# Performance work log

Hardware: AMD Instinct MI355X
Metric: run time of the kernel (lower is better)

The kernel has to match this reference:

```python
import jax, jax.numpy as jnp
import numpy as np

N = 50000   # nodes
E = 800000  # edges (before self-loops)
IN = 256    # in_dim
H = 4       # heads
C = 64      # out_dim per head
NEG_SLOPE = 0.2
BN_EPS = 1e-5


def setup_inputs() -> dict:
    key = jax.random.key(0)
    ks = jax.random.split(key, 6)
    feature = jax.random.normal(ks[0], (N, IN), jnp.float32)
    edge_index = jax.random.randint(ks[1], (2, E), 0, N, dtype=jnp.int64)
    W = jax.random.normal(ks[2], (IN, H * C), jnp.float32) * 0.05
    att_src = jax.random.normal(ks[3], (H, C), jnp.float32) * 0.1
    att_dst = jax.random.normal(ks[4], (H, C), jnp.float32) * 0.1
    bias = jnp.zeros((H * C,), jnp.float32)
    gamma = jnp.ones((H * C,), jnp.float32)
    beta = jnp.zeros((H * C,), jnp.float32)
    return {"feature": feature, "edge_index": edge_index, "W": W,
            "att_src": att_src, "att_dst": att_dst, "bias": bias,
            "gamma": gamma, "beta": beta}


def reference(feature, edge_index, W, att_src, att_dst, bias, gamma, beta):
    n = feature.shape[0]
    # linear projection -> [N, H, C]
    x = (feature @ W).reshape(n, H, C)
    # per-node attention logits [N, H]
    a_src = jnp.einsum('nhc,hc->nh', x, att_src)
    a_dst = jnp.einsum('nhc,hc->nh', x, att_dst)
    # add self loops (PyG GATConv default)
    loop = jnp.arange(n, dtype=edge_index.dtype)
    src = jnp.concatenate([edge_index[0], loop])
    dst = jnp.concatenate([edge_index[1], loop])
    # edge attention scores [E+N, H]
    e = jax.nn.leaky_relu(a_src[src] + a_dst[dst], NEG_SLOPE)
    # segment softmax over incoming edges of each dst node
    m = jax.ops.segment_max(e, dst, num_segments=n)
    ex = jnp.exp(e - m[dst])
    denom = jax.ops.segment_sum(ex, dst, num_segments=n)
    alpha = ex / denom[dst]                       # [E+N, H]
    # weighted message aggregation -> [N, H, C]
    msg = x[src] * alpha[:, :, None]
    out = jax.ops.segment_sum(msg, dst, num_segments=n)
    h = out.reshape(n, H * C) + bias
    # batchnorm over nodes (training-mode batch statistics)
    mu = jnp.mean(h, axis=0)
    var = jnp.var(h, axis=0)
    h = (h - mu) * jax.lax.rsqrt(var + BN_EPS) * gamma + beta
    # ELU activation
    h = jax.nn.elu(h)
    # residual (in_dim == out_dim * num_heads)
    return feature + h
```

## Files before the change

### kernel.cpp

```cpp
#include <hip/hip_runtime.h>

#define N_NODES 50000
#define N_EDGES 800000
#define NEG_SLOPE 0.2f
#define BN_EPS  1e-5f
#define LOG2E   1.44269504088896f

#define CHUNKS 256
#define EDGES_PER_CHUNK 3125
#define NCOARSE 1024
#define NBUCKET 782
#define GEMM_BLOCKS 782

typedef short bf16x8 __attribute__((ext_vector_type(8)));
typedef float floatx4 __attribute__((ext_vector_type(4)));

__device__ inline ushort f2bf(float f) {
    union { float f; unsigned u; } v; v.f = f;
    unsigned r = v.u + 0x7fff + ((v.u >> 16) & 1);
    return (ushort)(r >> 16);
}
__device__ inline float bf2f(ushort h) {
    union { unsigned u; float f; } v; v.u = ((unsigned)h) << 16;
    return v.f;
}

__global__ __launch_bounds__(256) void count_wt_kernel(const int* __restrict__ ei,
                                                       const float* __restrict__ W,
                                                       int* __restrict__ counts,
                                                       ushort* __restrict__ Wtb,
                                                       float* __restrict__ bnacc)
{
    __shared__ int hist[NCOARSE];
    const int t = threadIdx.x;
    const int b = blockIdx.x;
    if (b < CHUNKS) {
        for (int j = t; j < NCOARSE; j += 256) hist[j] = 0;
        __syncthreads();
        const int e0 = b * EDGES_PER_CHUNK;
        for (int e = e0 + t; e < e0 + EDGES_PER_CHUNK; e += 256)
            atomicAdd(&hist[ei[N_EDGES + e] >> 6], 1);
        __syncthreads();
        for (int j = t; j < NCOARSE; j += 256)
            counts[j * CHUNKS + b] = hist[j];
    } else {
        const int n = b - CHUNKS;
        Wtb[n * 256 + t] = f2bf(W[t * 256 + n]);
        if (n < 16) bnacc[n * 256 + t] = 0.f;
    }
}

__global__ __launch_bounds__(256) void sscan1_kernel(int* __restrict__ counts,
                                                     int* __restrict__ blocksum)
{
    __shared__ int sm[256];
    const int t = threadIdx.x;
    const int i = blockIdx.x * 256 + t;
    const int v = counts[i];
    sm[t] = v;
    __syncthreads();
#pragma unroll
    for (int off = 1; off < 256; off <<= 1) {
        const int u = (t >= off) ? sm[t - off] : 0;
        __syncthreads();
        sm[t] += u;
        __syncthreads();
    }
    counts[i] = sm[t] - v;
    if (t == 255) blocksum[blockIdx.x] = sm[255];
}

#define LDSTRIDE 40
__global__ __launch_bounds__(256) void scatter_gemm_kernel(const int* __restrict__ ei,
                                                           const int* __restrict__ counts,
                                                           const int* __restrict__ blocksum,
                                                           int* __restrict__ blockbase,
                                                           uint* __restrict__ tmp,
                                                           const float* __restrict__ A,
                                                           const ushort* __restrict__ Bt,
                                                           const float* __restrict__ att_src,
                                                           const float* __restrict__ att_dst,
                                                           ushort* __restrict__ Xb,
                                                           float* __restrict__ s,
                                                           float* __restrict__ d)
{
    __shared__ __align__(16) char smem[25600];
    const int tid = threadIdx.x;

    if (blockIdx.x < CHUNKS) {
        int* sm     = (int*)smem;
        int* bbase  = sm + 256;
        int* cursor = bbase + NCOARSE;
        const int t = tid;
        const int blk = blockIdx.x;

        int v[4], loc[4], tot = 0;
#pragma unroll
        for (int j = 0; j < 4; ++j) {
            v[j] = blocksum[t * 4 + j];
            loc[j] = tot;
            tot += v[j];
        }
        sm[t] = tot;
        __syncthreads();
#pragma unroll
        for (int off = 1; off < 256; off <<= 1) {
            const int u = (t >= off) ? sm[t - off] : 0;
            __syncthreads();
            sm[t] += u;
            __syncthreads();
        }
        const int base = sm[t] - tot;
#pragma unroll
        for (int j = 0; j < 4; ++j) bbase[t * 4 + j] = base + loc[j];
        if (blk == 0) {
#pragma unroll
            for (int j = 0; j < 4; ++j) blockbase[t * 4 + j] = base + loc[j];
        }
        __syncthreads();

        for (int u = t; u < NCOARSE; u += 256)
            cursor[u] = counts[u * CHUNKS + blk] + bbase[u];
        __syncthreads();
        const int e0 = blk * EDGES_PER_CHUNK;
        for (int e = e0 + t; e < e0 + EDGES_PER_CHUNK; e += 256) {
            const int src = ei[e];
            const int dst = ei[N_EDGES + e];
            const int pos = atomicAdd(&cursor[dst >> 6], 1);
            tmp[pos] = ((uint)src << 6) | (uint)(dst & 63);
        }
        return;
    }

    ushort* As = (ushort*)smem;
    ushort* Bs = As + 64 * LDSTRIDE;
    const int lane = tid & 63;
    const int wid = tid >> 6;
    const int row0 = (blockIdx.x - CHUNKS) * 64;
    const int quad = lane >> 4;
    const int l16  = lane & 15;

    floatx4 acc[4][4] = {};

    const int lr = tid >> 2;
    const int lk = (tid & 3) * 8;

    for (int k0 = 0; k0 < 256; k0 += 32) {
        {
            const int grow = row0 + lr;
            union { ushort u[8]; ulonglong2 v; } cv;
            if (grow < N_NODES) {
                const float4 f0 = *(const float4*)(A + (size_t)grow * 256 + k0 + lk);
                const float4 f1 = *(const float4*)(A + (size_t)grow * 256 + k0 + lk + 4);
                cv.u[0] = f2bf(f0.x); cv.u[1] = f2bf(f0.y);
                cv.u[2] = f2bf(f0.z); cv.u[3] = f2bf(f0.w);
                cv.u[4] = f2bf(f1.x); cv.u[5] = f2bf(f1.y);
                cv.u[6] = f2bf(f1.z); cv.u[7] = f2bf(f1.w);
            } else {
                cv.v = ulonglong2{0ull, 0ull};
            }
            *(ulonglong2*)(As + lr * LDSTRIDE + lk) = cv.v;
        }
#pragma unroll
        for (int r = 0; r < 4; ++r) {
            const int row = lr + r * 64;
            const ulonglong2 bv = *(const ulonglong2*)(Bt + (size_t)row * 256 + k0 + lk);
            *(ulonglong2*)(Bs + row * LDSTRIDE + lk) = bv;
        }
        __syncthreads();
        bf16x8 afrag[4], bfrag[4];
#pragma unroll
        for (int mi = 0; mi < 4; ++mi)
            afrag[mi] = *(const bf16x8*)(As + (mi * 16 + l16) * LDSTRIDE + quad * 8);
#pragma unroll
        for (int ni = 0; ni < 4; ++ni)
            bfrag[ni] = *(const bf16x8*)(Bs + (wid * 64 + ni * 16 + l16) * LDSTRIDE + quad * 8);
#pragma unroll
        for (int mi = 0; mi < 4; ++mi)
#pragma unroll
            for (int ni = 0; ni < 4; ++ni)
                acc[mi][ni] = __builtin_amdgcn_mfma_f32_16x16x32_bf16(afrag[mi], bfrag[ni], acc[mi][ni], 0, 0, 0);
        __syncthreads();
    }

    const int head = wid;
    float as_l[4], ad_l[4];
#pragma unroll
    for (int ni = 0; ni < 4; ++ni) {
        const int ch = head * 64 + ni * 16 + l16;
        as_l[ni] = att_src[ch];
        ad_l[ni] = att_dst[ch];
    }
#pragma unroll
    for (int mi = 0; mi < 4; ++mi) {
#pragma unroll
        for (int r = 0; r < 4; ++r) {
            const int grow = row0 + mi * 16 + quad * 4 + r;
            const bool ok = grow < N_NODES;
            float vs = 0.f, vd = 0.f;
            ushort4 o;
#pragma unroll
            for (int ni = 0; ni < 4; ++ni) {
                const float v = acc[mi][ni][r];
                vs += v * as_l[ni];
                vd += v * ad_l[ni];
                ((ushort*)&o)[ni] = f2bf(v);
            }
            if (ok)
                *(ushort4*)(Xb + (size_t)grow * 256 + head * 64 + l16 * 4) = o;
#pragma unroll
            for (int m = 8; m >= 1; m >>= 1) {
                vs += __shfl_xor(vs, m);
                vd += __shfl_xor(vd, m);
            }
            if (l16 == 0 && ok) {
                s[grow * 4 + head] = vs * LOG2E;
                d[grow * 4 + head] = vd * LOG2E;
            }
        }
    }
}

__global__ __launch_bounds__(256) void bucket_build_kernel(const uint* __restrict__ tmp,
                                                           const int* __restrict__ blockbase,
                                                           int* __restrict__ offsets,
                                                           int* __restrict__ csr_src)
{
    __shared__ int hist[64];
    __shared__ int sbuf[64];
    __shared__ int cursor[64];
    const int t = threadIdx.x;
    const int b = blockIdx.x;
    const int start = blockbase[b];
    const int end   = blockbase[b + 1];
    if (t < 64) hist[t] = 0;
    __syncthreads();
    for (int e = start + t; e < end; e += 256)
        atomicAdd(&hist[tmp[e] & 63], 1);
    __syncthreads();
    const int v = (t < 64) ? hist[t] : 0;
    if (t < 64) sbuf[t] = v;
    __syncthreads();
#pragma unroll
    for (int off = 1; off < 64; off <<= 1) {
        int u = 0;
        if (t < 64 && t >= off) u = sbuf[t - off];
        __syncthreads();
        if (t < 64) sbuf[t] += u;
        __syncthreads();
    }
    if (t < 64) {
        const int excl = start + sbuf[t] - v;
        cursor[t] = excl;
        const int node = b * 64 + t;
        if (node < N_NODES) offsets[node] = excl;
    }
    if (b == 0 && t == 0) offsets[N_NODES] = N_EDGES;
    __syncthreads();
    for (int e = start + t; e < end; e += 256) {
        const uint p = tmp[e];
        const int pos = atomicAdd(&cursor[p & 63], 1);
        csr_src[pos] = (int)(p >> 6);
    }
}

__global__ __launch_bounds__(256) void aggregate_kernel(const ushort* __restrict__ xb,
                                                        const float* __restrict__ s,
                                                        const float* __restrict__ d,
                                                        const int* __restrict__ offsets,
                                                        const int* __restrict__ csr_src,
                                                        ushort* __restrict__ hagg,
                                                        float* __restrict__ bnacc)
{
    __shared__ float bsum[4][256];
    __shared__ float bsq[4][256];
    const int wid = threadIdx.x >> 6;
    const int lane = threadIdx.x & 63;
    const int n = blockIdx.x * 4 + wid;
    const int h = lane >> 4;
    const float dn = d[n * 4 + h];
    const float sn = s[n * 4 + h];
    const ushort4 xr = *(const ushort4*)(xb + (size_t)n * 256 + lane * 4);
    float eself = sn + dn;
    eself = eself >= 0.f ? eself : NEG_SLOPE * eself;
    const float pself = exp2f(eself);
    float den = pself;
    float a0 = pself * bf2f(xr.x), a1 = pself * bf2f(xr.y);
    float a2 = pself * bf2f(xr.z), a3 = pself * bf2f(xr.w);
    const int e0 = __builtin_amdgcn_readfirstlane(offsets[n]);
    const int e1 = __builtin_amdgcn_readfirstlane(offsets[n + 1]);
    for (int e = e0; e < e1; e += 8) {
        int si[8];
        float lg[8];
        ushort4 xv[8];
#pragma unroll
        for (int j = 0; j < 8; ++j) {
            const int idx = e + j;
            const int idx2 = idx < e1 ? idx : e1 - 1;
            si[j] = __builtin_amdgcn_readfirstlane(csr_src[idx2]);
        }
#pragma unroll
        for (int j = 0; j < 8; ++j) lg[j] = s[si[j] * 4 + h] + dn;
#pragma unroll
        for (int j = 0; j < 8; ++j)
            xv[j] = *(const ushort4*)(xb + (size_t)si[j] * 256 + lane * 4);
#pragma unroll
        for (int j = 0; j < 8; ++j) {
            float l = (e + j < e1) ? lg[j] : -1e30f;
            l = l >= 0.f ? l : NEG_SLOPE * l;
            const float p = exp2f(l);
            den += p;
            a0 += p * bf2f(xv[j].x);
            a1 += p * bf2f(xv[j].y);
            a2 += p * bf2f(xv[j].z);
            a3 += p * bf2f(xv[j].w);
        }
    }
    const float inv = 1.0f / den;
    ushort4 o;
    o.x = f2bf(a0 * inv); o.y = f2bf(a1 * inv);
    o.z = f2bf(a2 * inv); o.w = f2bf(a3 * inv);
    *(ushort4*)(hagg + (size_t)n * 256 + lane * 4) = o;

    const float v0 = bf2f(o.x), v1 = bf2f(o.y), v2 = bf2f(o.z), v3 = bf2f(o.w);
    *(float4*)&bsum[wid][lane * 4] = float4{v0, v1, v2, v3};
    *(float4*)&bsq[wid][lane * 4]  = float4{v0 * v0, v1 * v1, v2 * v2, v3 * v3};
    __syncthreads();
    const int c = threadIdx.x;
    const float smv = bsum[0][c] + bsum[1][c] + bsum[2][c] + bsum[3][c];
    const float sqv = bsq[0][c]  + bsq[1][c]  + bsq[2][c]  + bsq[3][c];
    const int rep = (blockIdx.x & 7) * 256 + c;
    atomicAdd(&bnacc[rep], smv);
    atomicAdd(&bnacc[2048 + rep], sqv);
}

__global__ __launch_bounds__(256) void finalize_kernel(const float* __restrict__ feature,
                                                       const ushort* __restrict__ hagg,
                                                       const float* __restrict__ bnacc,
                                                       const float* __restrict__ gamma,
                                                       const float* __restrict__ beta,
                                                       float* __restrict__ out)
{
    __shared__ ushort hs[16][264];
    __shared__ float meanS[256], scaleS[256], betaS[256];
    const int t = threadIdx.x;
    const int wid = t >> 6;
    const int lane = t & 63;
    const int nbase = blockIdx.x * 16 + wid * 4;
    const int hblk = lane >> 4;
    const int l16 = lane & 15;

#pragma unroll
    for (int rr = 0; rr < 4; ++rr) {
        const int r = wid * 4 + rr;
        const int n = nbase + rr;
        const ushort4 hv = *(const ushort4*)(hagg + (size_t)n * 256 + lane * 4);
        hs[r][hblk * 64 + 0 * 16 + l16] = hv.x;
        hs[r][hblk * 64 + 1 * 16 + l16] = hv.y;
        hs[r][hblk * 64 + 2 * 16 + l16] = hv.z;
        hs[r][hblk * 64 + 3 * 16 + l16] = hv.w;
    }

    {
        float smv = 0.f, sqv = 0.f;
#pragma unroll
        for (int r = 0; r < 8; ++r) {
            smv += bnacc[r * 256 + t];
            sqv += bnacc[2048 + r * 256 + t];
        }
        const float m = smv * (1.0f / N_NODES);
        const float var = sqv * (1.0f / N_NODES) - m * m;
        const int w = t & 63;
        const int tc = (t >> 6) * 64 + (w & 3) * 16 + (w >> 2);
        meanS[tc] = m;
        scaleS[tc] = gamma[tc] * rsqrtf(var + BN_EPS);
        betaS[tc] = beta[tc];
    }
    __syncthreads();

#pragma unroll
    for (int rr = 0; rr < 4; ++rr) {
        const int r = wid * 4 + rr;
        const int n = nbase + rr;
        const ushort4 hv = *(const ushort4*)(&hs[r][lane * 4]);
        const float4 fv = *(const float4*)(feature + (size_t)n * 256 + lane * 4);
        const float hvf[4] = {bf2f(hv.x), bf2f(hv.y), bf2f(hv.z), bf2f(hv.w)};
        float4 o;
        float* op = (float*)&o;
        const float* fp = (const float*)&fv;
#pragma unroll
        for (int j = 0; j < 4; ++j) {
            const int ch = lane * 4 + j;
            float v = (hvf[j] - meanS[ch]) * scaleS[ch] + betaS[ch];
            v = v > 0.f ? v : exp2f(v * LOG2E) - 1.0f;
            op[j] = v + fp[j];
        }
        *(float4*)(out + (size_t)n * 256 + lane * 4) = o;
    }
}

extern "C" void kernel_launch(void* const* d_in, const int* in_sizes, int n_in,
                              void* d_out, int out_size, void* d_ws, size_t ws_size,
                              hipStream_t stream)
{
    const float* feature = (const float*)d_in[0];
    const int*   ei      = (const int*)d_in[1];
    const float* W       = (const float*)d_in[2];
    const float* att_src = (const float*)d_in[3];
    const float* att_dst = (const float*)d_in[4];
    const float* gamma   = (const float*)d_in[6];
    const float* beta    = (const float*)d_in[7];
    float* out = (float*)d_out;

    char* w = (char*)d_ws;
    auto carve = [&](size_t bytes) {
        char* p = w;
        w += (bytes + 255) & ~(size_t)255;
        return p;
    };
    ushort* Wtb      = (ushort*)carve((size_t)256 * 256 * 2);
    ushort* xb       = (ushort*)carve((size_t)N_NODES * 256 * 2);
    ushort* hagg     = (ushort*)carve((size_t)N_NODES * 256 * 2);
    float*  s        = (float*)carve((size_t)N_NODES * 4 * 4);
    float*  dv       = (float*)carve((size_t)N_NODES * 4 * 4);
    int*    counts   = (int*)carve((size_t)NCOARSE * CHUNKS * 4);
    int*    offsets  = (int*)carve((size_t)(N_NODES + 1) * 4);
    int*    csr_src  = (int*)carve((size_t)N_EDGES * 4);
    int*    blocksum = (int*)carve((size_t)NCOARSE * 4);
    int*    blockbase= (int*)carve((size_t)NCOARSE * 4);
    float*  bnacc    = (float*)carve((size_t)4096 * 4);
    uint*   tmp      = (uint*)hagg;

    count_wt_kernel<<<512, 256, 0, stream>>>(ei, W, counts, Wtb, bnacc);
    sscan1_kernel<<<NCOARSE, 256, 0, stream>>>(counts, blocksum);
    scatter_gemm_kernel<<<CHUNKS + GEMM_BLOCKS, 256, 0, stream>>>(
        ei, counts, blocksum, blockbase, tmp,
        feature, Wtb, att_src, att_dst, xb, s, dv);
    bucket_build_kernel<<<NBUCKET, 256, 0, stream>>>(tmp, blockbase, offsets, csr_src);
    aggregate_kernel<<<12500, 256, 0, stream>>>(xb, s, dv, offsets, csr_src, hagg, bnacc);
    finalize_kernel<<<3125, 256, 0, stream>>>(feature, hagg, bnacc, gamma, beta, out);
}
```

Baseline: 244.8 us.

## Replace counting-sort CSR build with fixed-capacity bucket slots and global atomics

Drops the histogram and scan kernels by scattering edges straight into fixed-size per-bucket slots (1280 entries per 64-node bucket) using global atomic cursors. Bucket build then sorts each slot in LDS in place and emits per-node start and end offsets, which the aggregation reads. This removes two launches and the count pass over the edge array, at the cost of global atomic contention. It also assumes no bucket ever receives more than 1280 edges, which holds for uniform random inputs but could overflow on skewed graphs.

Measured after the change: 398.5 us. 1.63x slower.

```diff
diff --git a/kernel.cpp b/kernel.cpp
--- a/kernel.cpp
+++ b/kernel.cpp
@@ -11,6 +11,7 @@
 #define NCOARSE 1024
 #define NBUCKET 782
 #define GEMM_BLOCKS 782
+#define SLOT 1280
 
 typedef short bf16x8 __attribute__((ext_vector_type(8)));
 typedef float floatx4 __attribute__((ext_vector_type(4)));
@@ -25,57 +26,22 @@
     return v.f;
 }
 
-__global__ __launch_bounds__(256) void count_wt_kernel(const int* __restrict__ ei,
-                                                       const float* __restrict__ W,
-                                                       int* __restrict__ counts,
-                                                       ushort* __restrict__ Wtb,
-                                                       float* __restrict__ bnacc)
-{
-    __shared__ int hist[NCOARSE];
+__global__ __launch_bounds__(256) void prep_kernel(const float* __restrict__ W,
+                                                   ushort* __restrict__ Wtb,
+                                                   float* __restrict__ bnacc,
+                                                   int* __restrict__ gcursor)
+{
     const int t = threadIdx.x;
-    const int b = blockIdx.x;
-    if (b < CHUNKS) {
-        for (int j = t; j < NCOARSE; j += 256) hist[j] = 0;
-        __syncthreads();
-        const int e0 = b * EDGES_PER_CHUNK;
-        for (int e = e0 + t; e < e0 + EDGES_PER_CHUNK; e += 256)
-            atomicAdd(&hist[ei[N_EDGES + e] >> 6], 1);
-        __syncthreads();
-        for (int j = t; j < NCOARSE; j += 256)
-            counts[j * CHUNKS + b] = hist[j];
-    } else {
-        const int n = b - CHUNKS;
-        Wtb[n * 256 + t] = f2bf(W[t * 256 + n]);
-        if (n < 16) bnacc[n * 256 + t] = 0.f;
-    }
-}
-
-__global__ __launch_bounds__(256) void sscan1_kernel(int* __restrict__ counts,
-                                                     int* __restrict__ blocksum)
-{
-    __shared__ int sm[256];
-    const int t = threadIdx.x;
-    const int i = blockIdx.x * 256 + t;
-    const int v = counts[i];
-    sm[t] = v;
-    __syncthreads();
-#pragma unroll
-    for (int off = 1; off < 256; off <<= 1) {
-        const int u = (t >= off) ? sm[t - off] : 0;
-        __syncthreads();
-        sm[t] += u;
-        __syncthreads();
-    }
-    counts[i] = sm[t] - v;
-    if (t == 255) blocksum[blockIdx.x] = sm[255];
+    const int n = blockIdx.x;
+    Wtb[n * 256 + t] = f2bf(W[t * 256 + n]);
+    if (n < 16) bnacc[n * 256 + t] = 0.f;
+    if (n >= 16 && n < 20) gcursor[(n - 16) * 256 + t] = 0;
 }
 
 #define LDSTRIDE 40
 __global__ __launch_bounds__(256) void scatter_gemm_kernel(const int* __restrict__ ei,
-                                                           const int* __restrict__ counts,
-                                                           const int* __restrict__ blocksum,
-                                                           int* __restrict__ blockbase,
-                                                           uint* __restrict__ tmp,
+                                                           int* __restrict__ gcursor,
+                                                           uint* __restrict__ slots,
                                                            const float* __restrict__ A,
                                                            const ushort* __restrict__ Bt,
                                                            const float* __restrict__ att_src,
@@ -88,46 +54,13 @@
     const int tid = threadIdx.x;
 
     if (blockIdx.x < CHUNKS) {
-        int* sm     = (int*)smem;
-        int* bbase  = sm + 256;
-        int* cursor = bbase + NCOARSE;
-        const int t = tid;
-        const int blk = blockIdx.x;
-
-        int v[4], loc[4], tot = 0;
-#pragma unroll
-        for (int j = 0; j < 4; ++j) {
-            v[j] = blocksum[t * 4 + j];
-            loc[j] = tot;
-            tot += v[j];
-        }
-        sm[t] = tot;
-        __syncthreads();
-#pragma unroll
-        for (int off = 1; off < 256; off <<= 1) {
-            const int u = (t >= off) ? sm[t - off] : 0;
-            __syncthreads();
-            sm[t] += u;
-            __syncthreads();
-        }
-        const int base = sm[t] - tot;
-#pragma unroll
-        for (int j = 0; j < 4; ++j) bbase[t * 4 + j] = base + loc[j];
-        if (blk == 0) {
-#pragma unroll
-            for (int j = 0; j < 4; ++j) blockbase[t * 4 + j] = base + loc[j];
-        }
-        __syncthreads();
-
-        for (int u = t; u < NCOARSE; u += 256)
-            cursor[u] = counts[u * CHUNKS + blk] + bbase[u];
-        __syncthreads();
-        const int e0 = blk * EDGES_PER_CHUNK;
-        for (int e = e0 + t; e < e0 + EDGES_PER_CHUNK; e += 256) {
+        const int e0 = blockIdx.x * EDGES_PER_CHUNK;
+        for (int e = e0 + tid; e < e0 + EDGES_PER_CHUNK; e += 256) {
             const int src = ei[e];
             const int dst = ei[N_EDGES + e];
-            const int pos = atomicAdd(&cursor[dst >> 6], 1);
-            tmp[pos] = ((uint)src << 6) | (uint)(dst & 63);
+            const int b = dst >> 6;
+            const int pos = atomicAdd(&gcursor[b], 1);
+            slots[b * SLOT + pos] = ((uint)src << 6) | (uint)(dst & 63);
         }
         return;
     }
@@ -221,22 +154,24 @@
     }
 }
 
-__global__ __launch_bounds__(256) void bucket_build_kernel(const uint* __restrict__ tmp,
-                                                           const int* __restrict__ blockbase,
+__global__ __launch_bounds__(256) void bucket_build_kernel(uint* __restrict__ slots,
+                                                           const int* __restrict__ gcursor,
                                                            int* __restrict__ offsets,
-                                                           int* __restrict__ csr_src)
-{
+                                                           int* __restrict__ ends)
+{
+    __shared__ uint ebuf[SLOT];
     __shared__ int hist[64];
     __shared__ int sbuf[64];
     __shared__ int cursor[64];
     const int t = threadIdx.x;
     const int b = blockIdx.x;
-    const int start = blockbase[b];
-    const int end   = blockbase[b + 1];
+    const int cnt = gcursor[b];
+    const int base = b * SLOT;
     if (t < 64) hist[t] = 0;
-    __syncthreads();
-    for (int e = start + t; e < end; e += 256)
-        atomicAdd(&hist[tmp[e] & 63], 1);
+    for (int e = t; e < cnt; e += 256) ebuf[e] = slots[base + e];
+    __syncthreads();
+    for (int e = t; e < cnt; e += 256)
+        atomicAdd(&hist[ebuf[e] & 63], 1);
     __syncthreads();
     const int v = (t < 64) ? hist[t] : 0;
     if (t < 64) sbuf[t] = v;
@@ -250,17 +185,19 @@
         __syncthreads();
     }
     if (t < 64) {
-        const int excl = start + sbuf[t] - v;
+        const int excl = sbuf[t] - v;
         cursor[t] = excl;
         const int node = b * 64 + t;
-        if (node < N_NODES) offsets[node] = excl;
-    }
-    if (b == 0 && t == 0) offsets[N_NODES] = N_EDGES;
-    __syncthreads();
-    for (int e = start + t; e < end; e += 256) {
-        const uint p = tmp[e];
+        if (node < N_NODES) {
+            offsets[node] = base + excl;
+            ends[node]    = base + excl + v;
+        }
+    }
+    __syncthreads();
+    for (int e = t; e < cnt; e += 256) {
+        const uint p = ebuf[e];
         const int pos = atomicAdd(&cursor[p & 63], 1);
-        csr_src[pos] = (int)(p >> 6);
+        slots[base + pos] = p >> 6;
     }
 }
 
@@ -268,7 +205,8 @@
                                                         const float* __restrict__ s,
                                                         const float* __restrict__ d,
                                                         const int* __restrict__ offsets,
-                                                        const int* __restrict__ csr_src,
+                                                        const int* __restrict__ ends,
+                                                        const uint* __restrict__ csr_src,
                                                         ushort* __restrict__ hagg,
                                                         float* __restrict__ bnacc)
 {
@@ -288,7 +226,7 @@
     float a0 = pself * bf2f(xr.x), a1 = pself * bf2f(xr.y);
     float a2 = pself * bf2f(xr.z), a3 = pself * bf2f(xr.w);
     const int e0 = __builtin_amdgcn_readfirstlane(offsets[n]);
-    const int e1 = __builtin_amdgcn_readfirstlane(offsets[n + 1]);
+    const int e1 = __builtin_amdgcn_readfirstlane(ends[n]);
     for (int e = e0; e < e1; e += 8) {
         int si[8];
         float lg[8];
@@ -297,7 +235,7 @@
         for (int j = 0; j < 8; ++j) {
             const int idx = e + j;
             const int idx2 = idx < e1 ? idx : e1 - 1;
-            si[j] = __builtin_amdgcn_readfirstlane(csr_src[idx2]);
+            si[j] = __builtin_amdgcn_readfirstlane((int)csr_src[idx2]);
         }
 #pragma unroll
         for (int j = 0; j < 8; ++j) lg[j] = s[si[j] * 4 + h] + dn;
@@ -423,20 +361,16 @@
     ushort* hagg     = (ushort*)carve((size_t)N_NODES * 256 * 2);
     float*  s        = (float*)carve((size_t)N_NODES * 4 * 4);
     float*  dv       = (float*)carve((size_t)N_NODES * 4 * 4);
-    int*    counts   = (int*)carve((size_t)NCOARSE * CHUNKS * 4);
-    int*    offsets  = (int*)carve((size_t)(N_NODES + 1) * 4);
-    int*    csr_src  = (int*)carve((size_t)N_EDGES * 4);
-    int*    blocksum = (int*)carve((size_t)NCOARSE * 4);
-    int*    blockbase= (int*)carve((size_t)NCOARSE * 4);
+    uint*   slots    = (uint*)carve((size_t)NCOARSE * SLOT * 4);
+    int*    offsets  = (int*)carve((size_t)N_NODES * 4);
+    int*    ends     = (int*)carve((size_t)N_NODES * 4);
+    int*    gcursor  = (int*)carve((size_t)NCOARSE * 4);
     float*  bnacc    = (float*)carve((size_t)4096 * 4);
-    uint*   tmp      = (uint*)hagg;
-
-    count_wt_kernel<<<512, 256, 0, stream>>>(ei, W, counts, Wtb, bnacc);
-    sscan1_kernel<<<NCOARSE, 256, 0, stream>>>(counts, blocksum);
+
+    prep_kernel<<<256, 256, 0, stream>>>(W, Wtb, bnacc, gcursor);
     scatter_gemm_kernel<<<CHUNKS + GEMM_BLOCKS, 256, 0, stream>>>(
-        ei, counts, blocksum, blockbase, tmp,
-        feature, Wtb, att_src, att_dst, xb, s, dv);
-    bucket_build_kernel<<<NBUCKET, 256, 0, stream>>>(tmp, blockbase, offsets, csr_src);
-    aggregate_kernel<<<12500, 256, 0, stream>>>(xb, s, dv, offsets, csr_src, hagg, bnacc);
+        ei, gcursor, slots, feature, Wtb, att_src, att_dst, xb, s, dv);
+    bucket_build_kernel<<<NBUCKET, 256, 0, stream>>>(slots, gcursor, offsets, ends);
+    aggregate_kernel<<<12500, 256, 0, stream>>>(xb, s, dv, offsets, ends, slots, hagg, bnacc);
     finalize_kernel<<<3125, 256, 0, stream>>>(feature, hagg, bnacc, gamma, beta, out);
 }
```

## Fuse per-bucket CSR build into aggregate kernel using shared-memory edge buffer

Applied to the files above, without the earlier changes.

Removes the separate bucket_build kernel and instead has each aggregate block load its 64-node bucket of packed edges, histogram and scatter them into a shared-memory buffer, then read source indices from LDS. This avoids writing and re-reading global offsets/csr_src arrays and one kernel launch. The tradeoff is that each bucket is re-sorted redundantly by the 16 blocks covering it, shared memory use grows, and a fixed buffer capacity (1344 edges, 6 per thread) risks overflow on skewed degree distributions.

Result: no change. 245.9 us (+0.5%).

```diff
diff --git a/kernel.cpp b/kernel.cpp
--- a/kernel.cpp
+++ b/kernel.cpp
@@ -9,8 +9,8 @@
 #define CHUNKS 256
 #define EDGES_PER_CHUNK 3125
 #define NCOARSE 1024
-#define NBUCKET 782
 #define GEMM_BLOCKS 782
+#define EBUF_CAP 1344
 
 typedef short bf16x8 __attribute__((ext_vector_type(8)));
 typedef float floatx4 __attribute__((ext_vector_type(4)));
@@ -221,63 +221,63 @@
     }
 }
 
-__global__ __launch_bounds__(256) void bucket_build_kernel(const uint* __restrict__ tmp,
-                                                           const int* __restrict__ blockbase,
-                                                           int* __restrict__ offsets,
-                                                           int* __restrict__ csr_src)
-{
-    __shared__ int hist[64];
-    __shared__ int sbuf[64];
-    __shared__ int cursor[64];
-    const int t = threadIdx.x;
-    const int b = blockIdx.x;
-    const int start = blockbase[b];
-    const int end   = blockbase[b + 1];
-    if (t < 64) hist[t] = 0;
-    __syncthreads();
-    for (int e = start + t; e < end; e += 256)
-        atomicAdd(&hist[tmp[e] & 63], 1);
-    __syncthreads();
-    const int v = (t < 64) ? hist[t] : 0;
-    if (t < 64) sbuf[t] = v;
-    __syncthreads();
-#pragma unroll
-    for (int off = 1; off < 64; off <<= 1) {
-        int u = 0;
-        if (t < 64 && t >= off) u = sbuf[t - off];
-        __syncthreads();
-        if (t < 64) sbuf[t] += u;
-        __syncthreads();
-    }
-    if (t < 64) {
-        const int excl = start + sbuf[t] - v;
-        cursor[t] = excl;
-        const int node = b * 64 + t;
-        if (node < N_NODES) offsets[node] = excl;
-    }
-    if (b == 0 && t == 0) offsets[N_NODES] = N_EDGES;
-    __syncthreads();
-    for (int e = start + t; e < end; e += 256) {
-        const uint p = tmp[e];
-        const int pos = atomicAdd(&cursor[p & 63], 1);
-        csr_src[pos] = (int)(p >> 6);
-    }
-}
-
 __global__ __launch_bounds__(256) void aggregate_kernel(const ushort* __restrict__ xb,
                                                         const float* __restrict__ s,
                                                         const float* __restrict__ d,
-                                                        const int* __restrict__ offsets,
-                                                        const int* __restrict__ csr_src,
+                                                        const uint* __restrict__ tmp,
+                                                        const int* __restrict__ blockbase,
                                                         ushort* __restrict__ hagg,
                                                         float* __restrict__ bnacc)
 {
+    __shared__ uint ebuf[EBUF_CAP];
+    __shared__ int hist[64];
+    __shared__ int nstart[64];
+    __shared__ int ncnt[64];
+    __shared__ int cur[64];
     __shared__ float bsum[4][256];
     __shared__ float bsq[4][256];
-    const int wid = threadIdx.x >> 6;
-    const int lane = threadIdx.x & 63;
+
+    const int t = threadIdx.x;
+    const int wid = t >> 6;
+    const int lane = t & 63;
+    const int h = lane >> 4;
+    const int bk = blockIdx.x >> 4;
+    const int gs = __builtin_amdgcn_readfirstlane(blockbase[bk]);
+    const int ge = __builtin_amdgcn_readfirstlane(blockbase[bk + 1]);
+    const int cnt = ge - gs;
+
+    if (t < 64) hist[t] = 0;
+    __syncthreads();
+    uint pr[6];
+    int npr = 0;
+    for (int e = t; e < cnt; e += 256) {
+        const uint p = tmp[gs + e];
+        pr[npr++] = p;
+        atomicAdd(&hist[p & 63], 1);
+    }
+    __syncthreads();
+    if (wid == 0) {
+        const int v = hist[lane];
+        int x = v;
+#pragma unroll
+        for (int off = 1; off < 64; off <<= 1) {
+            const int u = __shfl_up(x, off);
+            if (lane >= off) x += u;
+        }
+        nstart[lane] = x - v;
+        ncnt[lane] = v;
+        cur[lane] = x - v;
+    }
+    __syncthreads();
+    for (int k = 0; k < npr; ++k) {
+        const uint p = pr[k];
+        const int pos = atomicAdd(&cur[p & 63], 1);
+        ebuf[pos] = p >> 6;
+    }
+    __syncthreads();
+
     const int n = blockIdx.x * 4 + wid;
-    const int h = lane >> 4;
+    const int nl = n & 63;
     const float dn = d[n * 4 + h];
     const float sn = s[n * 4 + h];
     const ushort4 xr = *(const ushort4*)(xb + (size_t)n * 256 + lane * 4);
@@ -287,8 +287,8 @@
     float den = pself;
     float a0 = pself * bf2f(xr.x), a1 = pself * bf2f(xr.y);
     float a2 = pself * bf2f(xr.z), a3 = pself * bf2f(xr.w);
-    const int e0 = __builtin_amdgcn_readfirstlane(offsets[n]);
-    const int e1 = __builtin_amdgcn_readfirstlane(offsets[n + 1]);
+    const int e0 = __builtin_amdgcn_readfirstlane(nstart[nl]);
+    const int e1 = __builtin_amdgcn_readfirstlane(nstart[nl] + ncnt[nl]);
     for (int e = e0; e < e1; e += 8) {
         int si[8];
         float lg[8];
@@ -297,7 +297,7 @@
         for (int j = 0; j < 8; ++j) {
             const int idx = e + j;
             const int idx2 = idx < e1 ? idx : e1 - 1;
-            si[j] = __builtin_amdgcn_readfirstlane(csr_src[idx2]);
+            si[j] = __builtin_amdgcn_readfirstlane((int)ebuf[idx2]);
         }
 #pragma unroll
         for (int j = 0; j < 8; ++j) lg[j] = s[si[j] * 4 + h] + dn;
@@ -424,19 +424,16 @@
     float*  s        = (float*)carve((size_t)N_NODES * 4 * 4);
     float*  dv       = (float*)carve((size_t)N_NODES * 4 * 4);
     int*    counts   = (int*)carve((size_t)NCOARSE * CHUNKS * 4);
-    int*    offsets  = (int*)carve((size_t)(N_NODES + 1) * 4);
-    int*    csr_src  = (int*)carve((size_t)N_EDGES * 4);
+    uint*   tmp      = (uint*)carve((size_t)N_EDGES * 4);
     int*    blocksum = (int*)carve((size_t)NCOARSE * 4);
-    int*    blockbase= (int*)carve((size_t)NCOARSE * 4);
+    int*    blockbase= (int*)carve((size_t)(NCOARSE + 1) * 4);
     float*  bnacc    = (float*)carve((size_t)4096 * 4);
-    uint*   tmp      = (uint*)hagg;
 
     count_wt_kernel<<<512, 256, 0, stream>>>(ei, W, counts, Wtb, bnacc);
     sscan1_kernel<<<NCOARSE, 256, 0, stream>>>(counts, blocksum);
     scatter_gemm_kernel<<<CHUNKS + GEMM_BLOCKS, 256, 0, stream>>>(
         ei, counts, blocksum, blockbase, tmp,
         feature, Wtb, att_src, att_dst, xb, s, dv);
-    bucket_build_kernel<<<NBUCKET, 256, 0, stream>>>(tmp, blockbase, offsets, csr_src);
-    aggregate_kernel<<<12500, 256, 0, stream>>>(xb, s, dv, offsets, csr_src, hagg, bnacc);
+    aggregate_kernel<<<12500, 256, 0, stream>>>(xb, s, dv, tmp, blockbase, hagg, bnacc);
     finalize_kernel<<<3125, 256, 0, stream>>>(feature, hagg, bnacc, gamma, beta, out);
 }
```

## Split aggregation per node across two waves, each covering half the channels

Applied to the files above, without the earlier changes.

The aggregate kernel now uses two wavefronts per destination node, each handling two heads (128 channels) with 2 channels per lane, so the grid doubles to 25000 blocks. Block index is remapped so that blocks for the two halves of a node group are adjacent, which aims for cache reuse of the CSR indices and source rows. The intent is more memory-level parallelism and occupancy for the latency-bound gather. In exchange, CSR indices and logits are loaded twice, loads become narrower (4 bytes per lane), and BN atomics are issued by only half the threads of each block.

Result: slower. 259.8 us (+6.1%).

```diff
diff --git a/kernel.cpp b/kernel.cpp
--- a/kernel.cpp
+++ b/kernel.cpp
@@ -272,66 +272,70 @@
                                                         ushort* __restrict__ hagg,
                                                         float* __restrict__ bnacc)
 {
-    __shared__ float bsum[4][256];
-    __shared__ float bsq[4][256];
+    __shared__ float bsum[4][128];
+    __shared__ float bsq[4][128];
     const int wid = threadIdx.x >> 6;
     const int lane = threadIdx.x & 63;
-    const int n = blockIdx.x * 4 + wid;
-    const int h = lane >> 4;
+    const int x = blockIdx.x & 7;
+    const int j0 = blockIdx.x >> 3;
+    const int H = x >> 2;
+    const int nb = j0 * 4 + (x & 3);
+    const int n = nb * 4 + wid;
+    const int h = 2 * H + (lane >> 5);
+    const int cpos = H * 128 + lane * 2;
+
     const float dn = d[n * 4 + h];
     const float sn = s[n * 4 + h];
-    const ushort4 xr = *(const ushort4*)(xb + (size_t)n * 256 + lane * 4);
+    const ushort2 xr = *(const ushort2*)(xb + (size_t)n * 256 + cpos);
     float eself = sn + dn;
     eself = eself >= 0.f ? eself : NEG_SLOPE * eself;
     const float pself = exp2f(eself);
     float den = pself;
     float a0 = pself * bf2f(xr.x), a1 = pself * bf2f(xr.y);
-    float a2 = pself * bf2f(xr.z), a3 = pself * bf2f(xr.w);
     const int e0 = __builtin_amdgcn_readfirstlane(offsets[n]);
     const int e1 = __builtin_amdgcn_readfirstlane(offsets[n + 1]);
     for (int e = e0; e < e1; e += 8) {
         int si[8];
         float lg[8];
-        ushort4 xv[8];
-#pragma unroll
-        for (int j = 0; j < 8; ++j) {
-            const int idx = e + j;
+        ushort2 xv[8];
+#pragma unroll
+        for (int jj = 0; jj < 8; ++jj) {
+            const int idx = e + jj;
             const int idx2 = idx < e1 ? idx : e1 - 1;
-            si[j] = __builtin_amdgcn_readfirstlane(csr_src[idx2]);
-        }
-#pragma unroll
-        for (int j = 0; j < 8; ++j) lg[j] = s[si[j] * 4 + h] + dn;
-#pragma unroll
-        for (int j = 0; j < 8; ++j)
-            xv[j] = *(const ushort4*)(xb + (size_t)si[j] * 256 + lane * 4);
-#pragma unroll
-        for (int j = 0; j < 8; ++j) {
-            float l = (e + j < e1) ? lg[j] : -1e30f;
+            si[jj] = __builtin_amdgcn_readfirstlane(csr_src[idx2]);
+        }
+#pragma unroll
+        for (int jj = 0; jj < 8; ++jj) lg[jj] = s[si[jj] * 4 + h] + dn;
+#pragma unroll
+        for (int jj = 0; jj < 8; ++jj)
+            xv[jj] = *(const ushort2*)(xb + (size_t)si[jj] * 256 + cpos);
+#pragma unroll
+        for (int jj = 0; jj < 8; ++jj) {
+            float l = (e + jj < e1) ? lg[jj] : -1e30f;
             l = l >= 0.f ? l : NEG_SLOPE * l;
             const float p = exp2f(l);
             den += p;
-            a0 += p * bf2f(xv[j].x);
-            a1 += p * bf2f(xv[j].y);
-            a2 += p * bf2f(xv[j].z);
-            a3 += p * bf2f(xv[j].w);
+            a0 += p * bf2f(xv[jj].x);
+            a1 += p * bf2f(xv[jj].y);
         }
     }
     const float inv = 1.0f / den;
-    ushort4 o;
+    ushort2 o;
     o.x = f2bf(a0 * inv); o.y = f2bf(a1 * inv);
-    o.z = f2bf(a2 * inv); o.w = f2bf(a3 * inv);
-    *(ushort4*)(hagg + (size_t)n * 256 + lane * 4) = o;
-
-    const float v0 = bf2f(o.x), v1 = bf2f(o.y), v2 = bf2f(o.z), v3 = bf2f(o.w);
-    *(float4*)&bsum[wid][lane * 4] = float4{v0, v1, v2, v3};
-    *(float4*)&bsq[wid][lane * 4]  = float4{v0 * v0, v1 * v1, v2 * v2, v3 * v3};
-    __syncthreads();
-    const int c = threadIdx.x;
-    const float smv = bsum[0][c] + bsum[1][c] + bsum[2][c] + bsum[3][c];
-    const float sqv = bsq[0][c]  + bsq[1][c]  + bsq[2][c]  + bsq[3][c];
-    const int rep = (blockIdx.x & 7) * 256 + c;
-    atomicAdd(&bnacc[rep], smv);
-    atomicAdd(&bnacc[2048 + rep], sqv);
+    *(ushort2*)(hagg + (size_t)n * 256 + cpos) = o;
+
+    const float v0 = bf2f(o.x), v1 = bf2f(o.y);
+    *(float2*)&bsum[wid][lane * 2] = float2{v0, v1};
+    *(float2*)&bsq[wid][lane * 2]  = float2{v0 * v0, v1 * v1};
+    __syncthreads();
+    if (threadIdx.x < 128) {
+        const int c = threadIdx.x;
+        const float smv = bsum[0][c] + bsum[1][c] + bsum[2][c] + bsum[3][c];
+        const float sqv = bsq[0][c]  + bsq[1][c]  + bsq[2][c]  + bsq[3][c];
+        const int rep = x * 256 + H * 128 + c;
+        atomicAdd(&bnacc[rep], smv);
+        atomicAdd(&bnacc[2048 + rep], sqv);
+    }
 }
 
 __global__ __launch_bounds__(256) void finalize_kernel(const float* __restrict__ feature,
@@ -437,6 +441,6 @@
         ei, counts, blocksum, blockbase, tmp,
         feature, Wtb, att_src, att_dst, xb, s, dv);
     bucket_build_kernel<<<NBUCKET, 256, 0, stream>>>(tmp, blockbase, offsets, csr_src);
-    aggregate_kernel<<<12500, 256, 0, stream>>>(xb, s, dv, offsets, csr_src, hagg, bnacc);
+    aggregate_kernel<<<25000, 256, 0, stream>>>(xb, s, dv, offsets, csr_src, hagg, bnacc);
     finalize_kernel<<<3125, 256, 0, stream>>>(feature, hagg, bnacc, gamma, beta, out);
 }
```
